# Performance work log

Hardware: AMD Instinct MI355X
Metric: run time of the kernel (lower is better)

Reference implementation:

```python
import jax, jax.numpy as jnp
import numpy as np

D = 192          # embed_dim
DI = 2 * D       # d_inner (Mamba expand=2)
R = 12           # dt_rank = ceil(D / d_state)
N = 16           # d_state
DEPTH = 24
P = 16           # patch size
B = 4
SS, TS = 256, 128
PT = (TS // P) ** 2   # 64 template patches
PS = (SS // P) ** 2   # 256 search patches
L = PT + PS + 1       # 321 tokens (middle cls)


def setup_inputs() -> dict:
    key = jax.random.key(0)
    ks = jax.random.split(key, 24)
    f = lambda k, shp, s=0.02: (jax.random.normal(k, shp) * s).astype(jnp.float32)
    Alog = jnp.log(jnp.arange(1, N + 1, dtype=jnp.float32))  # S4D-real init
    Alog = jnp.tile(Alog, (DEPTH, DI, 1))
    return {
        "x_search": f(ks[0], (B, 3, SS, SS), 1.0),
        "x_template": f(ks[1], (B, 3, TS, TS), 1.0),
        "patch_w": f(ks[2], (D, 3, P, P)),
        "patch_b": jnp.zeros((D,), jnp.float32),
        "cls_token": f(ks[3], (1, 1, D)),
        "pos_embed": f(ks[4], (1, L, D)),
        "Win": f(ks[5], (DEPTH, 2 * DI, D)),
        "convw": f(ks[6], (DEPTH, DI, 4), 0.2),
        "convb": jnp.zeros((DEPTH, DI), jnp.float32),
        "Wx": f(ks[7], (DEPTH, R + 2 * N, DI)),
        "Wdt": f(ks[8], (DEPTH, DI, R), 0.1),
        "bdt": f(ks[9], (DEPTH, DI), 0.1),
        "Alog": Alog,
        "Dp": jnp.ones((DEPTH, DI), jnp.float32),
        "convw_b": f(ks[10], (DEPTH, DI, 4), 0.2),
        "convb_b": jnp.zeros((DEPTH, DI), jnp.float32),
        "Wx_b": f(ks[11], (DEPTH, R + 2 * N, DI)),
        "Wdt_b": f(ks[12], (DEPTH, DI, R), 0.1),
        "bdt_b": f(ks[13], (DEPTH, DI), 0.1),
        "Alog_b": Alog,
        "Dp_b": jnp.ones((DEPTH, DI), jnp.float32),
        "Wout": f(ks[14], (DEPTH, D, DI)),
        "normw": jnp.ones((DEPTH, D), jnp.float32),
        "normw_f": jnp.ones((D,), jnp.float32),
    }


def silu(x):
    return x * jax.nn.sigmoid(x)


def rmsnorm(x, w, eps=1e-5):
    return x * jax.lax.rsqrt(jnp.mean(x * x, -1, keepdims=True) + eps) * w


def patch_embed(x, w, b):
    # non-overlapping patch conv == blocked reshape + einsum
    Bn, C, H, W = x.shape
    xp = x.reshape(Bn, C, H // P, P, W // P, P)
    t = jnp.einsum('bcipjq,dcpq->bijd', xp, w)
    return t.reshape(Bn, (H // P) * (W // P), -1) + b


def causal_conv(u, w, b):
    # depthwise causal conv, kernel 4: u [B,DI,L], w [DI,4]
    Lx = u.shape[-1]
    up = jnp.pad(u, ((0, 0), (0, 0), (3, 0)))
    y = sum(w[:, k][None, :, None] * up[:, :, k:k + Lx] for k in range(4))
    return y + b[None, :, None]


def selective_scan(u, delta, A, Bm, Cm, Dp):
    # u, delta: [B,DI,L]; A: [DI,N]; Bm, Cm: [B,N,L]
    dA = jnp.exp(jnp.einsum('bdl,dn->lbdn', delta, A))
    dBu = jnp.einsum('bdl,bnl->lbdn', delta * u, Bm)

    def step(h, inp):
        dAt, dBut, ct = inp
        h = dAt * h + dBut
        return h, jnp.einsum('bdn,bn->bd', h, ct)

    h0 = jnp.zeros((u.shape[0], DI, N), u.dtype)
    _, ys = jax.lax.scan(step, h0, (dA, dBu, Cm.transpose(2, 0, 1)))
    y = ys.transpose(1, 2, 0)  # [B,DI,L]
    return y + Dp[None, :, None] * u


def _branch(x, z, convw, convb, Wx, Wdt, bdt, Alog, Dp):
    xc = silu(causal_conv(x, convw, convb))
    xdbl = jnp.einsum('bdl,ed->ble', xc, Wx)
    dt, Bm, Cm = xdbl[..., :R], xdbl[..., R:R + N], xdbl[..., R + N:]
    delta = jax.nn.softplus(jnp.einsum('blr,dr->bdl', dt, Wdt) + bdt[None, :, None])
    y = selective_scan(xc, delta, -jnp.exp(Alog), Bm.transpose(0, 2, 1),
                       Cm.transpose(0, 2, 1), Dp)
    return y * silu(z)


def _mixer(h, p):
    xz = jnp.einsum('bld,ed->ble', h, p['Win'])
    x = xz[..., :DI].transpose(0, 2, 1)   # [B,DI,L]
    z = xz[..., DI:].transpose(0, 2, 1)
    y = _branch(x, z, p['convw'], p['convb'], p['Wx'], p['Wdt'], p['bdt'],
                p['Alog'], p['Dp'])
    yb = _branch(x[..., ::-1], z[..., ::-1], p['convw_b'], p['convb_b'], p['Wx_b'],
                 p['Wdt_b'], p['bdt_b'], p['Alog_b'], p['Dp_b'])
    out = (y + yb[..., ::-1]) * 0.5  # bimamba v2 with if_divide_out
    return jnp.einsum('bdl,od->blo', out, p['Wout'])


def reference(x_search, x_template, patch_w, patch_b, cls_token, pos_embed,
              Win, convw, convb, Wx, Wdt, bdt, Alog, Dp,
              convw_b, convb_b, Wx_b, Wdt_b, bdt_b, Alog_b, Dp_b,
              Wout, normw, normw_f):
    ts = patch_embed(x_template, patch_w, patch_b)   # [B,64,D]
    ss = patch_embed(x_search, patch_w, patch_b)     # [B,256,D]
    tok = jnp.concatenate([ts, ss], 1)               # [B,320,D]
    mid = tok.shape[1] // 2
    cls = jnp.broadcast_to(cls_token, (tok.shape[0], 1, D))
    tok = jnp.concatenate([tok[:, :mid], cls, tok[:, mid:]], 1) + pos_embed

    lp = {'Win': Win, 'convw': convw, 'convb': convb, 'Wx': Wx, 'Wdt': Wdt,
          'bdt': bdt, 'Alog': Alog, 'Dp': Dp, 'convw_b': convw_b,
          'convb_b': convb_b, 'Wx_b': Wx_b, 'Wdt_b': Wdt_b, 'bdt_b': bdt_b,
          'Alog_b': Alog_b, 'Dp_b': Dp_b, 'Wout': Wout, 'normw': normw}

    def layer_step(carry, p):
        hidden, residual = carry
        residual = hidden + residual           # add
        hn = rmsnorm(residual, p['normw'])     # norm (fused_add_norm semantics)
        hidden = _mixer(hn, p)                 # mamba mixer
        return (hidden, residual), None

    (hidden, residual), _ = jax.lax.scan(layer_step, (tok, jnp.zeros_like(tok)), lp)
    return rmsnorm(hidden + residual, normw_f)   # final add + norm, [B,321,D]
```

## Files before the change

### kernel.cpp

```cpp
#include <hip/hip_runtime.h>
#include <math.h>

#define B_ 4
#define L_ 321
#define D_ 192
#define DI_ 384
#define E_ 768
#define R_ 12
#define N_ 16
#define DEPTH_ 24
#define XD 44

#define NC_ 21
#define LC_ 16

typedef __attribute__((ext_vector_type(8))) short bf16x8;
typedef __attribute__((ext_vector_type(4))) float f32x4;
typedef unsigned short ushort_t;

__device__ __forceinline__ float silu_f(float x) { return x / (1.f + __expf(-x)); }

__device__ __forceinline__ ushort_t f2bf(float x) {
    union { float f; unsigned u; } v; v.f = x;
    return (ushort_t)((v.u + 0x7fffu + ((v.u >> 16) & 1u)) >> 16);
}
__device__ __forceinline__ float bf2f(ushort_t h) {
    union { unsigned u; float f; } v; v.u = ((unsigned)h) << 16; return v.f;
}

__global__ void cvt_bf16(const float* __restrict__ src, ushort_t* __restrict__ dst, int n) {
    for (int i = blockIdx.x * blockDim.x + threadIdx.x; i < n; i += gridDim.x * blockDim.x)
        dst[i] = f2bf(src[i]);
}

__global__ void im2col_kernel(const float* __restrict__ xs, const float* __restrict__ xt,
                              ushort_t* __restrict__ pm) {
    int p_all = blockIdx.x % 320;
    int b = blockIdx.x / 320;
    const float* src; int i, j, W;
    if (p_all < 64) { int p = p_all; i = p >> 3; j = p & 7; W = 128; src = xt + (size_t)b*3*128*128; }
    else            { int p = p_all - 64; i = p >> 4; j = p & 15; W = 256; src = xs + (size_t)b*3*256*256; }
    ushort_t* dst = pm + (size_t)blockIdx.x * 768;
    for (int m = threadIdx.x; m < 768; m += blockDim.x) {
        int c = m >> 8, rem = m & 255, pp = rem >> 4, qq = rem & 15;
        dst[m] = f2bf(src[(size_t)(c*W + i*16 + pp)*W + j*16 + qq]);
    }
}

__global__ void tok_scatter(const float* __restrict__ tokmat, const float* __restrict__ pb,
                            const float* __restrict__ cls, const float* __restrict__ pos,
                            float* __restrict__ residual) {
    int blk = blockIdx.x;
    int b = blk / L_, t = blk % L_;
    int d = threadIdx.x;
    float v;
    if (t == 160) v = cls[d];
    else {
        int p = (t < 160) ? t : t - 1;
        v = tokmat[(size_t)(b*320 + p)*D_ + d] + pb[d];
    }
    residual[(size_t)(b*L_ + t)*D_ + d] = v + pos[t*D_ + d];
}

__global__ void rms0_kernel(const float* __restrict__ residual, const float* __restrict__ normw,
                            ushort_t* __restrict__ hn) {
    int row = blockIdx.x;
    int tid = threadIdx.x;
    __shared__ float red[256];
    float v = (tid < D_) ? residual[(size_t)row*D_ + tid] : 0.f;
    red[tid] = v * v;
    __syncthreads();
    for (int s = 128; s > 0; s >>= 1) { if (tid < s) red[tid] += red[tid + s]; __syncthreads(); }
    float scale = rsqrtf(red[0] / (float)D_ + 1e-5f);
    if (tid < D_) hn[(size_t)row*D_ + tid] = f2bf(v * scale * normw[tid]);
}

template<int WM, int WN, int MFR, int NFR>
__global__ __launch_bounds__(WM*WN*64) void mfma_gemm(const ushort_t* __restrict__ A,
                          const ushort_t* __restrict__ Bw, float* __restrict__ Cf,
                          int M, int N, int K) {
    constexpr int BM = WM * MFR * 16;
    constexpr int BN = WN * NFR * 16;
    int bx = blockIdx.x, by = blockIdx.y;
    int wave = threadIdx.x >> 6, lane = threadIdx.x & 63;
    int wr = wave / WN, wc = wave % WN;
    int m0 = by * BM + wr * MFR * 16;
    int n0 = bx * BN + wc * NFR * 16;
    int lrow = lane & 15;
    int lk   = (lane >> 4) * 8;

    f32x4 acc[MFR][NFR];
#pragma unroll
    for (int i = 0; i < MFR; ++i)
#pragma unroll
        for (int j = 0; j < NFR; ++j) acc[i][j] = (f32x4){0.f, 0.f, 0.f, 0.f};

    for (int k0 = 0; k0 < K; k0 += 32) {
        bf16x8 a[MFR], b[NFR];
#pragma unroll
        for (int i = 0; i < MFR; ++i) {
            int r = m0 + i*16 + lrow; r = min(r, M - 1);
            a[i] = *(const bf16x8*)(A + (size_t)r*K + k0 + lk);
        }
#pragma unroll
        for (int jn = 0; jn < NFR; ++jn) {
            int c = n0 + jn*16 + lrow; c = min(c, N - 1);
            b[jn] = *(const bf16x8*)(Bw + (size_t)c*K + k0 + lk);
        }
#pragma unroll
        for (int i = 0; i < MFR; ++i)
#pragma unroll
            for (int jn = 0; jn < NFR; ++jn)
                acc[i][jn] = __builtin_amdgcn_mfma_f32_16x16x32_bf16(a[i], b[jn], acc[i][jn], 0, 0, 0);
    }

    int crow = (lane >> 4) * 4;
    int ccol = lane & 15;
#pragma unroll
    for (int i = 0; i < MFR; ++i)
#pragma unroll
        for (int jn = 0; jn < NFR; ++jn) {
            int c = n0 + jn*16 + ccol;
            if (c >= N) continue;
#pragma unroll
            for (int j = 0; j < 4; ++j) {
                int r = m0 + i*16 + crow + j;
                if (r < M) Cf[(size_t)r*N + c] = acc[i][jn][j];
            }
        }
}

__global__ __launch_bounds__(256) void inproj_conv(
    const ushort_t* __restrict__ hn, const ushort_t* __restrict__ Win_l,
    const float* __restrict__ cw, const float* __restrict__ cb,
    const float* __restrict__ cwb, const float* __restrict__ cbb,
    ushort_t* __restrict__ xc_f, ushort_t* __restrict__ xc_b,
    ushort_t* __restrict__ zbuf) {
    int bx = blockIdx.x, by = blockIdx.y;
    int b = by / 6, lm0 = (by % 6) * 64;
    int wave = threadIdx.x >> 6, lane = threadIdx.x & 63;
    int lrow = lane & 15, lk = (lane >> 4) * 8;
    int ecol0 = bx * 64 + wave * 16;
    bool xp = bx < 6;
    int nf = xp ? 5 : 4;
    int lbase = xp ? lm0 - 3 : lm0;

    __shared__ float xt[80][68];

    f32x4 acc[5];
#pragma unroll
    for (int fi = 0; fi < 5; ++fi) acc[fi] = (f32x4){0.f, 0.f, 0.f, 0.f};

    for (int k0 = 0; k0 < D_; k0 += 32) {
        bf16x8 bw = *(const bf16x8*)(Win_l + (size_t)(ecol0 + lrow)*D_ + k0 + lk);
        for (int fi = 0; fi < nf; ++fi) {
            int l = lbase + fi*16 + lrow;
            l = min(max(l, 0), L_ - 1);
            bf16x8 af = *(const bf16x8*)(hn + (size_t)(b*L_ + l)*D_ + k0 + lk);
            acc[fi] = __builtin_amdgcn_mfma_f32_16x16x32_bf16(af, bw, acc[fi], 0, 0, 0);
        }
    }

    int crow = (lane >> 4) * 4, ccol = lane & 15;
    if (!xp) {
#pragma unroll
        for (int fi = 0; fi < 4; ++fi)
#pragma unroll
            for (int j = 0; j < 4; ++j) {
                int l = lm0 + fi*16 + crow + j;
                if (l < L_) zbuf[(size_t)(b*L_ + l)*DI_ + (ecol0 + ccol - DI_)] = f2bf(acc[fi][j]);
            }
        return;
    }
#pragma unroll
    for (int fi = 0; fi < 5; ++fi)
#pragma unroll
        for (int j = 0; j < 4; ++j)
            xt[fi*16 + crow + j][wave*16 + ccol] = acc[fi][j];
    __syncthreads();

    int dc = threadIdx.x & 63;
    int lofs = threadIdx.x >> 6;
    int d = bx*64 + dc;
    float4 wf = *(const float4*)(cw + (size_t)d*4);
    float4 wb = *(const float4*)(cwb + (size_t)d*4);
    float bf0 = cb[d], bb0 = cbb[d];
#pragma unroll
    for (int i = 0; i < 16; ++i) {
        int l2 = lofs + i*4;
        int lf = lm0 + l2;
        if (lf < L_) {
            float a0 = bf0;
#pragma unroll
            for (int k = 0; k < 4; ++k)
                if (lf - 3 + k >= 0) a0 = fmaf(((const float*)&wf)[k], xt[l2 + k][dc], a0);
            xc_f[(size_t)(b*L_ + lf)*DI_ + d] = f2bf(silu_f(a0));
        }
        int lpp = (L_ - 1) - lm0 - l2;
        if (lpp >= 0) {
            float a1 = bb0;
#pragma unroll
            for (int k = 0; k < 4; ++k)
                if (lpp - 3 + k >= 0) a1 = fmaf(((const float*)&wb)[k], xt[l2 + 6 - k][dc], a1);
            xc_b[(size_t)(b*L_ + lpp)*DI_ + d] = f2bf(silu_f(a1));
        }
    }
}

__global__ __launch_bounds__(64) void xdbl_dual(
    const ushort_t* __restrict__ xcf, const ushort_t* __restrict__ xcb,
    const ushort_t* __restrict__ Wxf, const ushort_t* __restrict__ Wxbw,
    float* __restrict__ xdf, float* __restrict__ xdb) {
    const int M = B_ * L_;
    int rev = blockIdx.y;
    const ushort_t* A  = rev ? xcb : xcf;
    const ushort_t* Bw = rev ? Wxbw : Wxf;
    float* C = rev ? xdb : xdf;
    int lane = threadIdx.x;
    int m0 = blockIdx.x * 16;
    int lrow = lane & 15, lk = (lane >> 4) * 8;

    f32x4 acc[3];
#pragma unroll
    for (int jn = 0; jn < 3; ++jn) acc[jn] = (f32x4){0.f, 0.f, 0.f, 0.f};

    for (int k0 = 0; k0 < DI_; k0 += 32) {
        int r = min(m0 + lrow, M - 1);
        bf16x8 a = *(const bf16x8*)(A + (size_t)r*DI_ + k0 + lk);
        bf16x8 b[3];
#pragma unroll
        for (int jn = 0; jn < 3; ++jn) {
            int c = min(jn*16 + lrow, XD - 1);
            b[jn] = *(const bf16x8*)(Bw + (size_t)c*DI_ + k0 + lk);
        }
#pragma unroll
        for (int jn = 0; jn < 3; ++jn)
            acc[jn] = __builtin_amdgcn_mfma_f32_16x16x32_bf16(a, b[jn], acc[jn], 0, 0, 0);
    }
    int crow = (lane >> 4) * 4, ccol = lane & 15;
#pragma unroll
    for (int jn = 0; jn < 3; ++jn) {
        int c = jn*16 + ccol;
        if (c >= XD) continue;
#pragma unroll
        for (int j = 0; j < 4; ++j) {
            int r = m0 + crow + j;
            if (r < M) C[(size_t)r*XD + c] = acc[jn][j];
        }
    }
}

template<bool LAST>
__global__ __launch_bounds__(256) void outproj_fused(
    const float* __restrict__ yf, const float* __restrict__ yb,
    const ushort_t* __restrict__ Ww,
    float* __restrict__ residual, const float* __restrict__ nw,
    ushort_t* __restrict__ hn, float* __restrict__ outp) {
    const int M = B_*L_, Nn = D_, K = DI_;
    int wave = threadIdx.x >> 6, lane = threadIdx.x & 63;
    int m0 = blockIdx.x * 16;
    int n0 = wave * 48;
    int lrow = lane & 15, lk = (lane >> 4) * 8;

    f32x4 acc[3];
#pragma unroll
    for (int jn = 0; jn < 3; ++jn) acc[jn] = (f32x4){0.f, 0.f, 0.f, 0.f};

    for (int k0 = 0; k0 < K; k0 += 32) {
        int r = min(m0 + lrow, M - 1);
        const float* p0 = yf + (size_t)r*K + k0 + lk;
        const float* p1 = yb + (size_t)r*K + k0 + lk;
        bf16x8 a;
#pragma unroll
        for (int j = 0; j < 8; ++j) a[j] = (short)f2bf(0.5f*(p0[j] + p1[j]));
        bf16x8 b[3];
#pragma unroll
        for (int jn = 0; jn < 3; ++jn) {
            int c = n0 + jn*16 + lrow;
            b[jn] = *(const bf16x8*)(Ww + (size_t)c*K + k0 + lk);
        }
#pragma unroll
        for (int jn = 0; jn < 3; ++jn)
            acc[jn] = __builtin_amdgcn_mfma_f32_16x16x32_bf16(a, b[jn], acc[jn], 0, 0, 0);
    }

    int crow = (lane >> 4) * 4, ccol = lane & 15;
    float resv[4][3];
    float sq[4] = {0.f, 0.f, 0.f, 0.f};
#pragma unroll
    for (int j = 0; j < 4; ++j) {
        int r = m0 + crow + j;
        bool ok = r < M;
#pragma unroll
        for (int jn = 0; jn < 3; ++jn) {
            int c = n0 + jn*16 + ccol;
            float v = ok ? (residual[(size_t)r*Nn + c] + acc[jn][j]) : 0.f;
            resv[j][jn] = v;
            sq[j] = fmaf(v, v, sq[j]);
        }
    }
#pragma unroll
    for (int m = 1; m < 16; m <<= 1)
#pragma unroll
        for (int j = 0; j < 4; ++j) sq[j] += __shfl_xor(sq[j], m, 64);

    __shared__ float part[16][4];
    if (ccol == 0) {
#pragma unroll
        for (int j = 0; j < 4; ++j) part[crow + j][wave] = sq[j];
    }
    __syncthreads();
#pragma unroll
    for (int j = 0; j < 4; ++j) {
        int r = m0 + crow + j;
        if (r >= M) continue;
        int rt = crow + j;
        float tot = part[rt][0] + part[rt][1] + part[rt][2] + part[rt][3];
        float scale = rsqrtf(tot / (float)Nn + 1e-5f);
#pragma unroll
        for (int jn = 0; jn < 3; ++jn) {
            int c = n0 + jn*16 + ccol;
            float v = resv[j][jn];
            if (LAST) {
                outp[(size_t)r*Nn + c] = v * scale * nw[c];
            } else {
                residual[(size_t)r*Nn + c] = v;
                hn[(size_t)r*Nn + c] = f2bf(v * scale * nw[c]);
            }
        }
    }
}

__global__ __launch_bounds__(192) void scan_part1(
                           const ushort_t* __restrict__ xc_f, const ushort_t* __restrict__ xc_b,
                           const float* __restrict__ xdbl_f, const float* __restrict__ xdbl_b,
                           const float* __restrict__ Wdt, const float* __restrict__ bdt,
                           const float* __restrict__ Wdtb, const float* __restrict__ bdtb,
                           const float* __restrict__ Alog, const float* __restrict__ Alogb,
                           float* __restrict__ hloc, float* __restrict__ aprod) {
    int c = blockIdx.x, b = blockIdx.y >> 1, half = blockIdx.y & 1, br = blockIdx.z;
    int tid = threadIdx.x;
    int d = half * 192 + tid;
    const ushort_t* xc = br ? xc_b : xc_f;
    const float* xd = br ? xdbl_b : xdbl_f;
    const float* Wd = br ? Wdtb : Wdt;
    const float* bd = br ? bdtb : bdt;
    const float* Al = br ? Alogb : Alog;
    __shared__ float sdt[LC_][R_];
    __shared__ float sB[LC_][N_];
    int lbeg = c * LC_;
    int len = min(lbeg + LC_, L_) - lbeg;
    for (int idx = tid; idx < len*N_; idx += 192) {
        int l2 = idx >> 4, n = idx & 15;
        sB[l2][n] = xd[((size_t)b*L_ + lbeg + l2)*XD + R_ + n];
    }
    for (int idx = tid; idx < len*R_; idx += 192) {
        int l2 = idx / R_, r = idx % R_;
        sdt[l2][r] = xd[((size_t)b*L_ + lbeg + l2)*XD + r];
    }
    __syncthreads();
    float wreg[R_];
#pragma unroll
    for (int r = 0; r < R_; ++r) wreg[r] = Wd[d*R_ + r];
    float bdv = bd[d];
    float a[N_];
#pragma unroll
    for (int n = 0; n < N_; ++n) a[n] = -__expf(Al[d*N_ + n]);
    float h[N_], ap[N_];
#pragma unroll
    for (int n = 0; n < N_; ++n) { h[n] = 0.f; ap[n] = 1.f; }

    auto step = [&](int l2, float u) {
        float dacc = bdv;
#pragma unroll
        for (int r = 0; r < R_; ++r) dacc = fmaf(wreg[r], sdt[l2][r], dacc);
        float dv = fmaxf(dacc, 0.f) + log1pf(__expf(-fabsf(dacc)));
        float du = dv * u;
#pragma unroll
        for (int n = 0; n < N_; ++n) {
            float e = __expf(dv * a[n]);
            h[n] = fmaf(e, h[n], du * sB[l2][n]);
            ap[n] *= e;
        }
    };
    if (len == LC_) {
        float u[LC_];
#pragma unroll
        for (int l2 = 0; l2 < LC_; ++l2)
            u[l2] = bf2f(xc[((size_t)b*L_ + lbeg + l2)*DI_ + d]);
#pragma unroll 4
        for (int l2 = 0; l2 < LC_; ++l2) step(l2, u[l2]);
    } else {
        for (int l2 = 0; l2 < len; ++l2)
            step(l2, bf2f(xc[((size_t)b*L_ + lbeg + l2)*DI_ + d]));
    }
    size_t base = (((size_t)(b*2 + br)*NC_ + c)*N_)*DI_ + d;
#pragma unroll
    for (int n = 0; n < N_; ++n) {
        hloc[base + (size_t)n*DI_]  = h[n];
        aprod[base + (size_t)n*DI_] = ap[n];
    }
}

__global__ void scan_combine(const float* __restrict__ hloc, const float* __restrict__ aprod,
                             float* __restrict__ hin) {
    int g = blockIdx.x * blockDim.x + threadIdx.x;
    int bb = g / (N_ * DI_);
    int rem = g % (N_ * DI_);
    float hrun = 0.f;
    for (int c = 0; c < NC_; ++c) {
        size_t idx = ((size_t)bb*NC_ + c)*N_*DI_ + rem;
        hin[idx] = hrun;
        hrun = fmaf(aprod[idx], hrun, hloc[idx]);
    }
}

__global__ __launch_bounds__(192) void scan_part3(
                           const ushort_t* __restrict__ xc_f, const ushort_t* __restrict__ xc_b,
                           const float* __restrict__ xdbl_f, const float* __restrict__ xdbl_b,
                           const float* __restrict__ Wdt, const float* __restrict__ bdt,
                           const float* __restrict__ Wdtb, const float* __restrict__ bdtb,
                           const ushort_t* __restrict__ zbuf,
                           const float* __restrict__ Alog, const float* __restrict__ Alogb,
                           const float* __restrict__ Dpf, const float* __restrict__ Dpb,
                           const float* __restrict__ hin,
                           float* __restrict__ y_f, float* __restrict__ y_b) {
    int c = blockIdx.x, b = blockIdx.y >> 1, half = blockIdx.y & 1, br = blockIdx.z;
    int tid = threadIdx.x;
    int d = half * 192 + tid;
    const ushort_t* xc = br ? xc_b : xc_f;
    const float* xd = br ? xdbl_b : xdbl_f;
    const float* Wd = br ? Wdtb : Wdt;
    const float* bd = br ? bdtb : bdt;
    const float* Al = br ? Alogb : Alog;
    const float* Dpp = br ? Dpb : Dpf;
    float* y = br ? y_b : y_f;
    __shared__ float sdt[LC_][R_];
    __shared__ float sB[LC_][N_];
    __shared__ float sC[LC_][N_];
    int lbeg = c * LC_;
    int len = min(lbeg + LC_, L_) - lbeg;
    for (int idx = tid; idx < len*N_; idx += 192) {
        int l2 = idx >> 4, n = idx & 15;
        size_t row = (size_t)b*L_ + lbeg + l2;
        sB[l2][n] = xd[row*XD + R_ + n];
        sC[l2][n] = xd[row*XD + R_ + N_ + n];
    }
    for (int idx = tid; idx < len*R_; idx += 192) {
        int l2 = idx / R_, r = idx % R_;
        sdt[l2][r] = xd[((size_t)b*L_ + lbeg + l2)*XD + r];
    }
    __syncthreads();
    float wreg[R_];
#pragma unroll
    for (int r = 0; r < R_; ++r) wreg[r] = Wd[d*R_ + r];
    float bdv = bd[d];
    float a[N_];
#pragma unroll
    for (int n = 0; n < N_; ++n) a[n] = -__expf(Al[d*N_ + n]);
    float h[N_];
    size_t hbase = (((size_t)(b*2 + br)*NC_ + c)*N_)*DI_ + d;
#pragma unroll
    for (int n = 0; n < N_; ++n) h[n] = hin[hbase + (size_t)n*DI_];
    float dpv = Dpp[d];

    auto step = [&](int l2, float u) {
        float dacc = bdv;
#pragma unroll
        for (int r = 0; r < R_; ++r) dacc = fmaf(wreg[r], sdt[l2][r], dacc);
        float dv = fmaxf(dacc, 0.f) + log1pf(__expf(-fabsf(dacc)));
        float du = dv * u;
        float yv = 0.f;
#pragma unroll
        for (int n = 0; n < N_; ++n) {
            float e = __expf(dv * a[n]);
            h[n] = fmaf(e, h[n], du * sB[l2][n]);
            yv = fmaf(h[n], sC[l2][n], yv);
        }
        yv = fmaf(dpv, u, yv);
        int lo = br ? (L_ - 1 - (lbeg + l2)) : (lbeg + l2);
        float zv = bf2f(zbuf[((size_t)b*L_ + lo)*DI_ + d]);
        y[((size_t)b*L_ + lo)*DI_ + d] = yv * silu_f(zv);
    };
    if (len == LC_) {
        float u[LC_];
#pragma unroll
        for (int l2 = 0; l2 < LC_; ++l2)
            u[l2] = bf2f(xc[((size_t)b*L_ + lbeg + l2)*DI_ + d]);
#pragma unroll 4
        for (int l2 = 0; l2 < LC_; ++l2) step(l2, u[l2]);
    } else {
        for (int l2 = 0; l2 < len; ++l2)
            step(l2, bf2f(xc[((size_t)b*L_ + lbeg + l2)*DI_ + d]));
    }
}

extern "C" void kernel_launch(void* const* d_in, const int* in_sizes, int n_in,
                              void* d_out, int out_size, void* d_ws, size_t ws_size,
                              hipStream_t stream) {
    const float* xs     = (const float*)d_in[0];
    const float* xt     = (const float*)d_in[1];
    const float* pw     = (const float*)d_in[2];
    const float* pb     = (const float*)d_in[3];
    const float* cls    = (const float*)d_in[4];
    const float* pos    = (const float*)d_in[5];
    const float* Win    = (const float*)d_in[6];
    const float* convw  = (const float*)d_in[7];
    const float* convb  = (const float*)d_in[8];
    const float* Wx     = (const float*)d_in[9];
    const float* Wdt    = (const float*)d_in[10];
    const float* bdt    = (const float*)d_in[11];
    const float* Alog   = (const float*)d_in[12];
    const float* Dp     = (const float*)d_in[13];
    const float* convwb = (const float*)d_in[14];
    const float* convbb = (const float*)d_in[15];
    const float* Wxb    = (const float*)d_in[16];
    const float* Wdtb   = (const float*)d_in[17];
    const float* bdtb   = (const float*)d_in[18];
    const float* Alogb  = (const float*)d_in[19];
    const float* Dpb    = (const float*)d_in[20];
    const float* Wout   = (const float*)d_in[21];
    const float* normw  = (const float*)d_in[22];
    const float* normwf = (const float*)d_in[23];
    float* out = (float*)d_out;

    float* ws = (float*)d_ws;
    size_t off = 0;
    auto alloc = [&](size_t nfloats) { float* p = ws + off; off += nfloats; return p; };
    const size_t BL = (size_t)B_ * L_;
    const size_t CHNK = (size_t)B_ * 2 * NC_ * N_ * DI_;

    float*    residual = alloc(BL * D_);
    ushort_t* hn_bf    = (ushort_t*)alloc(BL * D_ / 2);
    ushort_t* zbuf     = (ushort_t*)alloc(BL * DI_ / 2);
    ushort_t* xcf_bf   = (ushort_t*)alloc(BL * DI_ / 2);
    ushort_t* xcb_bf   = (ushort_t*)alloc(BL * DI_ / 2);
    float*    xdbl_f   = alloc(BL * XD);
    float*    xdbl_b   = alloc(BL * XD);
    float*    y_f      = alloc(BL * DI_);
    float*    y_b      = alloc(BL * DI_);
    float*    hloc     = alloc(CHNK);
    float*    aprod    = alloc(CHNK);
    float*    hin      = alloc(CHNK);
    ushort_t* pw_bf    = (ushort_t*)alloc((size_t)D_ * 768 / 2);
    ushort_t* Win_bf   = (ushort_t*)alloc((size_t)DEPTH_ * E_ * D_ / 2);
    ushort_t* Wx_bf    = (ushort_t*)alloc((size_t)DEPTH_ * XD * DI_ / 2);
    ushort_t* Wxb_bf   = (ushort_t*)alloc((size_t)DEPTH_ * XD * DI_ / 2);
    ushort_t* Wout_bf  = (ushort_t*)alloc((size_t)DEPTH_ * D_ * DI_ / 2);
    (void)ws_size; (void)in_sizes; (void)n_in; (void)out_size;

    cvt_bf16<<<dim3(64),   dim3(256), 0, stream>>>(pw,   pw_bf,   D_ * 768);
    cvt_bf16<<<dim3(2048), dim3(256), 0, stream>>>(Win,  Win_bf,  DEPTH_ * E_ * D_);
    cvt_bf16<<<dim3(512),  dim3(256), 0, stream>>>(Wx,   Wx_bf,   DEPTH_ * XD * DI_);
    cvt_bf16<<<dim3(512),  dim3(256), 0, stream>>>(Wxb,  Wxb_bf,  DEPTH_ * XD * DI_);
    cvt_bf16<<<dim3(1024), dim3(256), 0, stream>>>(Wout, Wout_bf, DEPTH_ * D_ * DI_);

    ushort_t* pmat   = (ushort_t*)y_f;
    float*    tokmat = y_b;
    im2col_kernel<<<dim3(B_ * 320), dim3(256), 0, stream>>>(xs, xt, pmat);
    mfma_gemm<2, 2, 2, 2><<<dim3(3, 20), dim3(256), 0, stream>>>(
        pmat, pw_bf, tokmat, B_ * 320, D_, 768);
    tok_scatter<<<dim3(B_ * L_), dim3(192), 0, stream>>>(tokmat, pb, cls, pos, residual);
    rms0_kernel<<<dim3((int)BL), dim3(256), 0, stream>>>(residual, normw, hn_bf);

    for (int layer = 0; layer < DEPTH_; ++layer) {
        const ushort_t* Win_l  = Win_bf  + (size_t)layer * E_ * D_;
        const ushort_t* Wx_l   = Wx_bf   + (size_t)layer * XD * DI_;
        const ushort_t* Wxb_l  = Wxb_bf  + (size_t)layer * XD * DI_;
        const ushort_t* Wout_l = Wout_bf + (size_t)layer * D_ * DI_;
        const float* cw_l    = convw  + (size_t)layer * DI_ * 4;
        const float* cb_l    = convb  + (size_t)layer * DI_;
        const float* cwb_l   = convwb + (size_t)layer * DI_ * 4;
        const float* cbb_l   = convbb + (size_t)layer * DI_;
        const float* Wdt_l   = Wdt    + (size_t)layer * DI_ * R_;
        const float* Wdtb_l  = Wdtb   + (size_t)layer * DI_ * R_;
        const float* bdt_l   = bdt    + (size_t)layer * DI_;
        const float* bdtb_l  = bdtb   + (size_t)layer * DI_;
        const float* Alog_l  = Alog   + (size_t)layer * DI_ * N_;
        const float* Alogb_l = Alogb  + (size_t)layer * DI_ * N_;
        const float* Dp_l    = Dp     + (size_t)layer * DI_;
        const float* Dpb_l   = Dpb    + (size_t)layer * DI_;

        inproj_conv<<<dim3(12, 24), dim3(256), 0, stream>>>(
            hn_bf, Win_l, cw_l, cb_l, cwb_l, cbb_l, xcf_bf, xcb_bf, zbuf);
        xdbl_dual<<<dim3(81, 2), dim3(64), 0, stream>>>(
            xcf_bf, xcb_bf, Wx_l, Wxb_l, xdbl_f, xdbl_b);
        scan_part1<<<dim3(NC_, B_ * 2, 2), dim3(192), 0, stream>>>(
            xcf_bf, xcb_bf, xdbl_f, xdbl_b, Wdt_l, bdt_l, Wdtb_l, bdtb_l,
            Alog_l, Alogb_l, hloc, aprod);
        scan_combine<<<dim3((B_*2*N_*DI_)/256), dim3(256), 0, stream>>>(hloc, aprod, hin);
        scan_part3<<<dim3(NC_, B_ * 2, 2), dim3(192), 0, stream>>>(
            xcf_bf, xcb_bf, xdbl_f, xdbl_b, Wdt_l, bdt_l, Wdtb_l, bdtb_l, zbuf,
            Alog_l, Alogb_l, Dp_l, Dpb_l, hin, y_f, y_b);
        if (layer < DEPTH_ - 1) {
            outproj_fused<false><<<dim3(81), dim3(256), 0, stream>>>(
                y_f, y_b, Wout_l, residual, normw + (size_t)(layer + 1) * D_, hn_bf, nullptr);
        } else {
            outproj_fused<true><<<dim3(81), dim3(256), 0, stream>>>(
                y_f, y_b, Wout_l, residual, normwf, nullptr, out);
        }
    }
}
```

Measured before the change: 2.040 ms.

## Split in_proj and conv into generic GEMM plus conv; fuse x_proj into scan part 1

```diff
diff --git a/kernel.cpp b/kernel.cpp
--- a/kernel.cpp
+++ b/kernel.cpp
@@ -75,9 +75,10 @@
     if (tid < D_) hn[(size_t)row*D_ + tid] = f2bf(v * scale * normw[tid]);
 }
 
-template<int WM, int WN, int MFR, int NFR>
+template<int WM, int WN, int MFR, int NFR, int CMODE>
 __global__ __launch_bounds__(WM*WN*64) void mfma_gemm(const ushort_t* __restrict__ A,
-                          const ushort_t* __restrict__ Bw, float* __restrict__ Cf,
+                          const ushort_t* __restrict__ Bw,
+                          float* __restrict__ Cf, ushort_t* __restrict__ Ch,
                           int M, int N, int K) {
     constexpr int BM = WM * MFR * 16;
     constexpr int BN = WN * NFR * 16;
@@ -125,240 +126,88 @@
 #pragma unroll
             for (int j = 0; j < 4; ++j) {
                 int r = m0 + i*16 + crow + j;
-                if (r < M) Cf[(size_t)r*N + c] = acc[i][jn][j];
+                if (r < M) {
+                    if (CMODE == 0) Cf[(size_t)r*N + c] = acc[i][jn][j];
+                    else            Ch[(size_t)r*N + c] = f2bf(acc[i][jn][j]);
+                }
             }
         }
 }
 
-__global__ __launch_bounds__(256) void inproj_conv(
-    const ushort_t* __restrict__ hn, const ushort_t* __restrict__ Win_l,
-    const float* __restrict__ cw, const float* __restrict__ cb,
-    const float* __restrict__ cwb, const float* __restrict__ cbb,
-    ushort_t* __restrict__ xc_f, ushort_t* __restrict__ xc_b,
-    ushort_t* __restrict__ zbuf) {
-    int bx = blockIdx.x, by = blockIdx.y;
-    int b = by / 6, lm0 = (by % 6) * 64;
-    int wave = threadIdx.x >> 6, lane = threadIdx.x & 63;
-    int lrow = lane & 15, lk = (lane >> 4) * 8;
-    int ecol0 = bx * 64 + wave * 16;
-    bool xp = bx < 6;
-    int nf = xp ? 5 : 4;
-    int lbase = xp ? lm0 - 3 : lm0;
-
-    __shared__ float xt[80][68];
-
-    f32x4 acc[5];
-#pragma unroll
-    for (int fi = 0; fi < 5; ++fi) acc[fi] = (f32x4){0.f, 0.f, 0.f, 0.f};
-
-    for (int k0 = 0; k0 < D_; k0 += 32) {
-        bf16x8 bw = *(const bf16x8*)(Win_l + (size_t)(ecol0 + lrow)*D_ + k0 + lk);
-        for (int fi = 0; fi < nf; ++fi) {
-            int l = lbase + fi*16 + lrow;
-            l = min(max(l, 0), L_ - 1);
-            bf16x8 af = *(const bf16x8*)(hn + (size_t)(b*L_ + l)*D_ + k0 + lk);
-            acc[fi] = __builtin_amdgcn_mfma_f32_16x16x32_bf16(af, bw, acc[fi], 0, 0, 0);
-        }
-    }
-
-    int crow = (lane >> 4) * 4, ccol = lane & 15;
-    if (!xp) {
-#pragma unroll
-        for (int fi = 0; fi < 4; ++fi)
-#pragma unroll
-            for (int j = 0; j < 4; ++j) {
-                int l = lm0 + fi*16 + crow + j;
-                if (l < L_) zbuf[(size_t)(b*L_ + l)*DI_ + (ecol0 + ccol - DI_)] = f2bf(acc[fi][j]);
-            }
-        return;
-    }
-#pragma unroll
-    for (int fi = 0; fi < 5; ++fi)
-#pragma unroll
-        for (int j = 0; j < 4; ++j)
-            xt[fi*16 + crow + j][wave*16 + ccol] = acc[fi][j];
-    __syncthreads();
-
-    int dc = threadIdx.x & 63;
-    int lofs = threadIdx.x >> 6;
-    int d = bx*64 + dc;
-    float4 wf = *(const float4*)(cw + (size_t)d*4);
-    float4 wb = *(const float4*)(cwb + (size_t)d*4);
-    float bf0 = cb[d], bb0 = cbb[d];
-#pragma unroll
-    for (int i = 0; i < 16; ++i) {
-        int l2 = lofs + i*4;
-        int lf = lm0 + l2;
-        if (lf < L_) {
-            float a0 = bf0;
-#pragma unroll
-            for (int k = 0; k < 4; ++k)
-                if (lf - 3 + k >= 0) a0 = fmaf(((const float*)&wf)[k], xt[l2 + k][dc], a0);
-            xc_f[(size_t)(b*L_ + lf)*DI_ + d] = f2bf(silu_f(a0));
-        }
-        int lpp = (L_ - 1) - lm0 - l2;
-        if (lpp >= 0) {
-            float a1 = bb0;
-#pragma unroll
-            for (int k = 0; k < 4; ++k)
-                if (lpp - 3 + k >= 0) a1 = fmaf(((const float*)&wb)[k], xt[l2 + 6 - k][dc], a1);
-            xc_b[(size_t)(b*L_ + lpp)*DI_ + d] = f2bf(silu_f(a1));
-        }
-    }
-}
-
-__global__ __launch_bounds__(64) void xdbl_dual(
-    const ushort_t* __restrict__ xcf, const ushort_t* __restrict__ xcb,
+__global__ void conv_kernel(const ushort_t* __restrict__ xz,
+                            const float* __restrict__ cw, const float* __restrict__ cb,
+                            const float* __restrict__ cwb, const float* __restrict__ cbb,
+                            ushort_t* __restrict__ xc_f, ushort_t* __restrict__ xc_b) {
+    int blk = blockIdx.x;
+    int b = blk / L_, l = blk % L_;
+    int d = threadIdx.x;
+    const ushort_t* xbase = xz + (size_t)b*L_*E_ + d;
+    float acc = cb[d];
+#pragma unroll
+    for (int k = 0; k < 4; ++k) {
+        int t = l - 3 + k;
+        if (t >= 0) acc = fmaf(cw[d*4 + k], bf2f(xbase[(size_t)t*E_]), acc);
+    }
+    xc_f[(size_t)(b*L_ + l)*DI_ + d] = f2bf(silu_f(acc));
+    float accb = cbb[d];
+#pragma unroll
+    for (int k = 0; k < 4; ++k) {
+        int t = l - 3 + k;
+        if (t >= 0) accb = fmaf(cwb[d*4 + k], bf2f(xbase[(size_t)(L_ - 1 - t)*E_]), accb);
+    }
+    xc_b[(size_t)(b*L_ + l)*DI_ + d] = f2bf(silu_f(accb));
+}
+
+__global__ __launch_bounds__(384) void scan1_xdbl(
+    const ushort_t* __restrict__ xc_f, const ushort_t* __restrict__ xc_b,
     const ushort_t* __restrict__ Wxf, const ushort_t* __restrict__ Wxbw,
-    float* __restrict__ xdf, float* __restrict__ xdb) {
-    const int M = B_ * L_;
-    int rev = blockIdx.y;
-    const ushort_t* A  = rev ? xcb : xcf;
-    const ushort_t* Bw = rev ? Wxbw : Wxf;
-    float* C = rev ? xdb : xdf;
-    int lane = threadIdx.x;
-    int m0 = blockIdx.x * 16;
-    int lrow = lane & 15, lk = (lane >> 4) * 8;
-
-    f32x4 acc[3];
-#pragma unroll
-    for (int jn = 0; jn < 3; ++jn) acc[jn] = (f32x4){0.f, 0.f, 0.f, 0.f};
-
-    for (int k0 = 0; k0 < DI_; k0 += 32) {
-        int r = min(m0 + lrow, M - 1);
-        bf16x8 a = *(const bf16x8*)(A + (size_t)r*DI_ + k0 + lk);
-        bf16x8 b[3];
-#pragma unroll
-        for (int jn = 0; jn < 3; ++jn) {
-            int c = min(jn*16 + lrow, XD - 1);
-            b[jn] = *(const bf16x8*)(Bw + (size_t)c*DI_ + k0 + lk);
-        }
-#pragma unroll
-        for (int jn = 0; jn < 3; ++jn)
-            acc[jn] = __builtin_amdgcn_mfma_f32_16x16x32_bf16(a, b[jn], acc[jn], 0, 0, 0);
-    }
-    int crow = (lane >> 4) * 4, ccol = lane & 15;
-#pragma unroll
-    for (int jn = 0; jn < 3; ++jn) {
-        int c = jn*16 + ccol;
-        if (c >= XD) continue;
-#pragma unroll
-        for (int j = 0; j < 4; ++j) {
-            int r = m0 + crow + j;
-            if (r < M) C[(size_t)r*XD + c] = acc[jn][j];
-        }
-    }
-}
-
-template<bool LAST>
-__global__ __launch_bounds__(256) void outproj_fused(
-    const float* __restrict__ yf, const float* __restrict__ yb,
-    const ushort_t* __restrict__ Ww,
-    float* __restrict__ residual, const float* __restrict__ nw,
-    ushort_t* __restrict__ hn, float* __restrict__ outp) {
-    const int M = B_*L_, Nn = D_, K = DI_;
-    int wave = threadIdx.x >> 6, lane = threadIdx.x & 63;
-    int m0 = blockIdx.x * 16;
-    int n0 = wave * 48;
-    int lrow = lane & 15, lk = (lane >> 4) * 8;
-
-    f32x4 acc[3];
-#pragma unroll
-    for (int jn = 0; jn < 3; ++jn) acc[jn] = (f32x4){0.f, 0.f, 0.f, 0.f};
-
-    for (int k0 = 0; k0 < K; k0 += 32) {
-        int r = min(m0 + lrow, M - 1);
-        const float* p0 = yf + (size_t)r*K + k0 + lk;
-        const float* p1 = yb + (size_t)r*K + k0 + lk;
-        bf16x8 a;
-#pragma unroll
-        for (int j = 0; j < 8; ++j) a[j] = (short)f2bf(0.5f*(p0[j] + p1[j]));
-        bf16x8 b[3];
-#pragma unroll
-        for (int jn = 0; jn < 3; ++jn) {
-            int c = n0 + jn*16 + lrow;
-            b[jn] = *(const bf16x8*)(Ww + (size_t)c*K + k0 + lk);
-        }
-#pragma unroll
-        for (int jn = 0; jn < 3; ++jn)
-            acc[jn] = __builtin_amdgcn_mfma_f32_16x16x32_bf16(a, b[jn], acc[jn], 0, 0, 0);
-    }
-
-    int crow = (lane >> 4) * 4, ccol = lane & 15;
-    float resv[4][3];
-    float sq[4] = {0.f, 0.f, 0.f, 0.f};
-#pragma unroll
-    for (int j = 0; j < 4; ++j) {
-        int r = m0 + crow + j;
-        bool ok = r < M;
-#pragma unroll
-        for (int jn = 0; jn < 3; ++jn) {
-            int c = n0 + jn*16 + ccol;
-            float v = ok ? (residual[(size_t)r*Nn + c] + acc[jn][j]) : 0.f;
-            resv[j][jn] = v;
-            sq[j] = fmaf(v, v, sq[j]);
-        }
-    }
-#pragma unroll
-    for (int m = 1; m < 16; m <<= 1)
-#pragma unroll
-        for (int j = 0; j < 4; ++j) sq[j] += __shfl_xor(sq[j], m, 64);
-
-    __shared__ float part[16][4];
-    if (ccol == 0) {
-#pragma unroll
-        for (int j = 0; j < 4; ++j) part[crow + j][wave] = sq[j];
-    }
-    __syncthreads();
-#pragma unroll
-    for (int j = 0; j < 4; ++j) {
-        int r = m0 + crow + j;
-        if (r >= M) continue;
-        int rt = crow + j;
-        float tot = part[rt][0] + part[rt][1] + part[rt][2] + part[rt][3];
-        float scale = rsqrtf(tot / (float)Nn + 1e-5f);
-#pragma unroll
-        for (int jn = 0; jn < 3; ++jn) {
-            int c = n0 + jn*16 + ccol;
-            float v = resv[j][jn];
-            if (LAST) {
-                outp[(size_t)r*Nn + c] = v * scale * nw[c];
-            } else {
-                residual[(size_t)r*Nn + c] = v;
-                hn[(size_t)r*Nn + c] = f2bf(v * scale * nw[c]);
-            }
-        }
-    }
-}
-
-__global__ __launch_bounds__(192) void scan_part1(
-                           const ushort_t* __restrict__ xc_f, const ushort_t* __restrict__ xc_b,
-                           const float* __restrict__ xdbl_f, const float* __restrict__ xdbl_b,
-                           const float* __restrict__ Wdt, const float* __restrict__ bdt,
-                           const float* __restrict__ Wdtb, const float* __restrict__ bdtb,
-                           const float* __restrict__ Alog, const float* __restrict__ Alogb,
-                           float* __restrict__ hloc, float* __restrict__ aprod) {
-    int c = blockIdx.x, b = blockIdx.y >> 1, half = blockIdx.y & 1, br = blockIdx.z;
-    int tid = threadIdx.x;
-    int d = half * 192 + tid;
+    const float* __restrict__ Wdt, const float* __restrict__ bdt,
+    const float* __restrict__ Wdtb, const float* __restrict__ bdtb,
+    const float* __restrict__ Alog, const float* __restrict__ Alogb,
+    float* __restrict__ xdbl_f, float* __restrict__ xdbl_b,
+    float* __restrict__ hloc, float* __restrict__ aprod) {
+    int c = blockIdx.x, b = blockIdx.y, br = blockIdx.z;
+    int tid = threadIdx.x, wave = tid >> 6, lane = tid & 63;
     const ushort_t* xc = br ? xc_b : xc_f;
-    const float* xd = br ? xdbl_b : xdbl_f;
+    const ushort_t* Wx = br ? Wxbw : Wxf;
     const float* Wd = br ? Wdtb : Wdt;
     const float* bd = br ? bdtb : bdt;
     const float* Al = br ? Alogb : Alog;
-    __shared__ float sdt[LC_][R_];
-    __shared__ float sB[LC_][N_];
+    float* xdout = br ? xdbl_b : xdbl_f;
+
+    __shared__ float sxd[LC_][48];
     int lbeg = c * LC_;
     int len = min(lbeg + LC_, L_) - lbeg;
-    for (int idx = tid; idx < len*N_; idx += 192) {
-        int l2 = idx >> 4, n = idx & 15;
-        sB[l2][n] = xd[((size_t)b*L_ + lbeg + l2)*XD + R_ + n];
-    }
-    for (int idx = tid; idx < len*R_; idx += 192) {
-        int l2 = idx / R_, r = idx % R_;
-        sdt[l2][r] = xd[((size_t)b*L_ + lbeg + l2)*XD + r];
+
+    if (wave < 3) {
+        int lrow = lane & 15, lk = (lane >> 4) * 8;
+        int arow = b * L_ + min(lbeg + lrow, L_ - 1);
+        int bcol = min(wave * 16 + lrow, XD - 1);
+        f32x4 acc = (f32x4){0.f, 0.f, 0.f, 0.f};
+        for (int k0 = 0; k0 < DI_; k0 += 32) {
+            bf16x8 a  = *(const bf16x8*)(xc + (size_t)arow * DI_ + k0 + lk);
+            bf16x8 bw = *(const bf16x8*)(Wx + (size_t)bcol * DI_ + k0 + lk);
+            acc = __builtin_amdgcn_mfma_f32_16x16x32_bf16(a, bw, acc, 0, 0, 0);
+        }
+        int crow = (lane >> 4) * 4, ccol = lane & 15;
+#pragma unroll
+        for (int j = 0; j < 4; ++j) sxd[crow + j][wave * 16 + ccol] = acc[j];
+    }
+
+    int d = tid;
+    float u[LC_];
+    if (len == LC_) {
+#pragma unroll
+        for (int l2 = 0; l2 < LC_; ++l2)
+            u[l2] = bf2f(xc[((size_t)b*L_ + lbeg + l2)*DI_ + d]);
     }
     __syncthreads();
+
+    for (int idx = tid; idx < len * XD; idx += 384) {
+        int l2 = idx / XD, col = idx % XD;
+        xdout[((size_t)b*L_ + lbeg + l2)*XD + col] = sxd[l2][col];
+    }
+
     float wreg[R_];
 #pragma unroll
     for (int r = 0; r < R_; ++r) wreg[r] = Wd[d*R_ + r];
@@ -370,24 +219,20 @@
 #pragma unroll
     for (int n = 0; n < N_; ++n) { h[n] = 0.f; ap[n] = 1.f; }
 
-    auto step = [&](int l2, float u) {
+    auto step = [&](int l2, float uv) {
         float dacc = bdv;
 #pragma unroll
-        for (int r = 0; r < R_; ++r) dacc = fmaf(wreg[r], sdt[l2][r], dacc);
+        for (int r = 0; r < R_; ++r) dacc = fmaf(wreg[r], sxd[l2][r], dacc);
         float dv = fmaxf(dacc, 0.f) + log1pf(__expf(-fabsf(dacc)));
-        float du = dv * u;
+        float du = dv * uv;
 #pragma unroll
         for (int n = 0; n < N_; ++n) {
             float e = __expf(dv * a[n]);
-            h[n] = fmaf(e, h[n], du * sB[l2][n]);
+            h[n] = fmaf(e, h[n], du * sxd[l2][R_ + n]);
             ap[n] *= e;
         }
     };
     if (len == LC_) {
-        float u[LC_];
-#pragma unroll
-        for (int l2 = 0; l2 < LC_; ++l2)
-            u[l2] = bf2f(xc[((size_t)b*L_ + lbeg + l2)*DI_ + d]);
 #pragma unroll 4
         for (int l2 = 0; l2 < LC_; ++l2) step(l2, u[l2]);
     } else {
@@ -420,7 +265,7 @@
                            const float* __restrict__ xdbl_f, const float* __restrict__ xdbl_b,
                            const float* __restrict__ Wdt, const float* __restrict__ bdt,
                            const float* __restrict__ Wdtb, const float* __restrict__ bdtb,
-                           const ushort_t* __restrict__ zbuf,
+                           const ushort_t* __restrict__ xz,
                            const float* __restrict__ Alog, const float* __restrict__ Alogb,
                            const float* __restrict__ Dpf, const float* __restrict__ Dpb,
                            const float* __restrict__ hin,
@@ -464,12 +309,12 @@
     for (int n = 0; n < N_; ++n) h[n] = hin[hbase + (size_t)n*DI_];
     float dpv = Dpp[d];
 
-    auto step = [&](int l2, float u) {
+    auto step = [&](int l2, float uv) {
         float dacc = bdv;
 #pragma unroll
         for (int r = 0; r < R_; ++r) dacc = fmaf(wreg[r], sdt[l2][r], dacc);
         float dv = fmaxf(dacc, 0.f) + log1pf(__expf(-fabsf(dacc)));
-        float du = dv * u;
+        float du = dv * uv;
         float yv = 0.f;
 #pragma unroll
         for (int n = 0; n < N_; ++n) {
@@ -477,9 +322,9 @@
             h[n] = fmaf(e, h[n], du * sB[l2][n]);
             yv = fmaf(h[n], sC[l2][n], yv);
         }
-        yv = fmaf(dpv, u, yv);
+        yv = fmaf(dpv, uv, yv);
         int lo = br ? (L_ - 1 - (lbeg + l2)) : (lbeg + l2);
-        float zv = bf2f(zbuf[((size_t)b*L_ + lo)*DI_ + d]);
+        float zv = bf2f(xz[((size_t)b*L_ + lo)*E_ + DI_ + d]);
         y[((size_t)b*L_ + lo)*DI_ + d] = yv * silu_f(zv);
     };
     if (len == LC_) {
@@ -492,6 +337,87 @@
     } else {
         for (int l2 = 0; l2 < len; ++l2)
             step(l2, bf2f(xc[((size_t)b*L_ + lbeg + l2)*DI_ + d]));
+    }
+}
+
+template<bool LAST>
+__global__ __launch_bounds__(256) void outproj_fused(
+    const float* __restrict__ yf, const float* __restrict__ yb,
+    const ushort_t* __restrict__ Ww,
+    float* __restrict__ residual, const float* __restrict__ nw,
+    ushort_t* __restrict__ hn, float* __restrict__ outp) {
+    const int M = B_*L_, Nn = D_, K = DI_;
+    int wave = threadIdx.x >> 6, lane = threadIdx.x & 63;
+    int m0 = blockIdx.x * 16;
+    int n0 = wave * 48;
+    int lrow = lane & 15, lk = (lane >> 4) * 8;
+
+    f32x4 acc[3];
+#pragma unroll
+    for (int jn = 0; jn < 3; ++jn) acc[jn] = (f32x4){0.f, 0.f, 0.f, 0.f};
+
+    for (int k0 = 0; k0 < K; k0 += 32) {
+        int r = min(m0 + lrow, M - 1);
+        const float* p0 = yf + (size_t)r*K + k0 + lk;
+        const float* p1 = yb + (size_t)r*K + k0 + lk;
+        bf16x8 a;
+#pragma unroll
+        for (int j = 0; j < 8; ++j) a[j] = (short)f2bf(0.5f*(p0[j] + p1[j]));
+        bf16x8 b[3];
+#pragma unroll
+        for (int jn = 0; jn < 3; ++jn) {
+            int c = n0 + jn*16 + lrow;
+            b[jn] = *(const bf16x8*)(Ww + (size_t)c*K + k0 + lk);
+        }
+#pragma unroll
+        for (int jn = 0; jn < 3; ++jn)
+            acc[jn] = __builtin_amdgcn_mfma_f32_16x16x32_bf16(a, b[jn], acc[jn], 0, 0, 0);
+    }
+
+    int crow = (lane >> 4) * 4, ccol = lane & 15;
+    float resv[4][3];
+    float sq[4] = {0.f, 0.f, 0.f, 0.f};
+#pragma unroll
+    for (int j = 0; j < 4; ++j) {
+        int r = m0 + crow + j;
+        bool ok = r < M;
+#pragma unroll
+        for (int jn = 0; jn < 3; ++jn) {
+            int c = n0 + jn*16 + ccol;
+            float v = ok ? (residual[(size_t)r*Nn + c] + acc[jn][j]) : 0.f;
+            resv[j][jn] = v;
+            sq[j] = fmaf(v, v, sq[j]);
+        }
+    }
+#pragma unroll
+    for (int m = 1; m < 16; m <<= 1)
+#pragma unroll
+        for (int j = 0; j < 4; ++j) sq[j] += __shfl_xor(sq[j], m, 64);
+
+    __shared__ float part[16][4];
+    if (ccol == 0) {
+#pragma unroll
+        for (int j = 0; j < 4; ++j) part[crow + j][wave] = sq[j];
+    }
+    __syncthreads();
+#pragma unroll
+    for (int j = 0; j < 4; ++j) {
+        int r = m0 + crow + j;
+        if (r >= M) continue;
+        int rt = crow + j;
+        float tot = part[rt][0] + part[rt][1] + part[rt][2] + part[rt][3];
+        float scale = rsqrtf(tot / (float)Nn + 1e-5f);
+#pragma unroll
+        for (int jn = 0; jn < 3; ++jn) {
+            int c = n0 + jn*16 + ccol;
+            float v = resv[j][jn];
+            if (LAST) {
+                outp[(size_t)r*Nn + c] = v * scale * nw[c];
+            } else {
+                residual[(size_t)r*Nn + c] = v;
+                hn[(size_t)r*Nn + c] = f2bf(v * scale * nw[c]);
+            }
+        }
     }
 }
 
@@ -532,7 +458,7 @@
 
     float*    residual = alloc(BL * D_);
     ushort_t* hn_bf    = (ushort_t*)alloc(BL * D_ / 2);
-    ushort_t* zbuf     = (ushort_t*)alloc(BL * DI_ / 2);
+    ushort_t* xzb_bf   = (ushort_t*)alloc(BL * E_ / 2);
     ushort_t* xcf_bf   = (ushort_t*)alloc(BL * DI_ / 2);
     ushort_t* xcb_bf   = (ushort_t*)alloc(BL * DI_ / 2);
     float*    xdbl_f   = alloc(BL * XD);
@@ -558,8 +484,8 @@
     ushort_t* pmat   = (ushort_t*)y_f;
     float*    tokmat = y_b;
     im2col_kernel<<<dim3(B_ * 320), dim3(256), 0, stream>>>(xs, xt, pmat);
-    mfma_gemm<2, 2, 2, 2><<<dim3(3, 20), dim3(256), 0, stream>>>(
-        pmat, pw_bf, tokmat, B_ * 320, D_, 768);
+    mfma_gemm<2, 2, 2, 2, 0><<<dim3(3, 20), dim3(256), 0, stream>>>(
+        pmat, pw_bf, tokmat, nullptr, B_ * 320, D_, 768);
     tok_scatter<<<dim3(B_ * L_), dim3(192), 0, stream>>>(tokmat, pb, cls, pos, residual);
     rms0_kernel<<<dim3((int)BL), dim3(256), 0, stream>>>(residual, normw, hn_bf);
 
@@ -581,16 +507,16 @@
         const float* Dp_l    = Dp     + (size_t)layer * DI_;
         const float* Dpb_l   = Dpb    + (size_t)layer * DI_;
 
-        inproj_conv<<<dim3(12, 24), dim3(256), 0, stream>>>(
-            hn_bf, Win_l, cw_l, cb_l, cwb_l, cbb_l, xcf_bf, xcb_bf, zbuf);
-        xdbl_dual<<<dim3(81, 2), dim3(64), 0, stream>>>(
-            xcf_bf, xcb_bf, Wx_l, Wxb_l, xdbl_f, xdbl_b);
-        scan_part1<<<dim3(NC_, B_ * 2, 2), dim3(192), 0, stream>>>(
-            xcf_bf, xcb_bf, xdbl_f, xdbl_b, Wdt_l, bdt_l, Wdtb_l, bdtb_l,
-            Alog_l, Alogb_l, hloc, aprod);
+        mfma_gemm<2, 2, 2, 2, 1><<<dim3(12, 21), dim3(256), 0, stream>>>(
+            hn_bf, Win_l, nullptr, xzb_bf, (int)BL, E_, D_);
+        conv_kernel<<<dim3((int)BL), dim3(DI_), 0, stream>>>(
+            xzb_bf, cw_l, cb_l, cwb_l, cbb_l, xcf_bf, xcb_bf);
+        scan1_xdbl<<<dim3(NC_, B_, 2), dim3(384), 0, stream>>>(
+            xcf_bf, xcb_bf, Wx_l, Wxb_l, Wdt_l, bdt_l, Wdtb_l, bdtb_l,
+            Alog_l, Alogb_l, xdbl_f, xdbl_b, hloc, aprod);
         scan_combine<<<dim3((B_*2*N_*DI_)/256), dim3(256), 0, stream>>>(hloc, aprod, hin);
         scan_part3<<<dim3(NC_, B_ * 2, 2), dim3(192), 0, stream>>>(
-            xcf_bf, xcb_bf, xdbl_f, xdbl_b, Wdt_l, bdt_l, Wdtb_l, bdtb_l, zbuf,
+            xcf_bf, xcb_bf, xdbl_f, xdbl_b, Wdt_l, bdt_l, Wdtb_l, bdtb_l, xzb_bf,
             Alog_l, Alogb_l, Dp_l, Dpb_l, hin, y_f, y_b);
         if (layer < DEPTH_ - 1) {
             outproj_fused<false><<<dim3(81), dim3(256), 0, stream>>>(
```

Result: faster. 1.831 ms (-10.2%).
